# Kernel tuning notes

Measured on AMD Instinct MI355X. Metric: run time of the kernel, lower is better.

## Reference

```python
import jax, jax.numpy as jnp
import numpy as np

B, N, S, C1, C2, CIN, CO = 16, 4096, 1024, 128, 256, 384, 128
BN_EPS = 1e-5


def _bn(x, g, b):
    # BatchNorm1d in training mode: biased batch stats over (B, L) per channel.
    m = x.mean(axis=(0, 1))
    v = x.var(axis=(0, 1))
    return (x - m) * jax.lax.rsqrt(v + BN_EPS) * g + b


def _gelu(x):
    return jax.nn.gelu(x, approximate=False)  # torch nn.GELU default (erf)


def _conv1x1(x, w, b):
    # x: (B, L, Cin), w: (Cout, Cin) -> (B, L, Cout)
    return jnp.einsum('blc,oc->blo', x, w) + b


def setup_inputs() -> dict:
    ks = jax.random.split(jax.random.key(0), 20)
    sc = 0.05
    return {
        'xyz1': jax.random.normal(ks[0], (B, N, 3), jnp.float32),
        'xyz2': jax.random.normal(ks[1], (B, S, 3), jnp.float32),
        'points1': jax.random.normal(ks[2], (B, N, C1), jnp.float32),
        'points2': jax.random.normal(ks[3], (B, S, C2), jnp.float32),
        'fuse_w': jax.random.normal(ks[4], (CO, CIN), jnp.float32) * sc,
        'fuse_b': jax.random.normal(ks[5], (CO,), jnp.float32) * sc,
        'fuse_g': jnp.ones((CO,), jnp.float32),
        'fuse_bt': jnp.zeros((CO,), jnp.float32),
        'w1': jax.random.normal(ks[6], (CO, CO), jnp.float32) * sc,
        'b1': jax.random.normal(ks[7], (CO,), jnp.float32) * sc,
        'g1': jnp.ones((CO,), jnp.float32),
        'bt1': jnp.zeros((CO,), jnp.float32),
        'w2': jax.random.normal(ks[8], (CO, CO), jnp.float32) * sc,
        'b2': jax.random.normal(ks[9], (CO,), jnp.float32) * sc,
        'g2': jnp.ones((CO,), jnp.float32),
        'bt2': jnp.zeros((CO,), jnp.float32),
    }


def reference(xyz1, xyz2, points1, points2,
              fuse_w, fuse_b, fuse_g, fuse_bt,
              w1, b1, g1, bt1, w2, b2, g2, bt2):
    # pairwise euclidean distances (B, N, S) without (B,N,S,3) intermediate
    sq = (jnp.sum(xyz1 * xyz1, -1)[:, :, None]
          + jnp.sum(xyz2 * xyz2, -1)[:, None, :]
          - 2.0 * jnp.einsum('bnd,bsd->bns', xyz1, xyz2))
    dists = jnp.sqrt(jnp.maximum(sq, 1e-12))
    # 3 nearest neighbors, ascending distance
    neg_d3, idx = jax.lax.top_k(-dists, 3)        # (B, N, 3)
    d3 = -neg_d3
    dist_recip = 1.0 / (d3 + 1e-8)
    weight = dist_recip / jnp.sum(dist_recip, axis=-1, keepdims=True)
    gathered = points2[jnp.arange(B)[:, None, None], idx]  # (B, N, 3, C2)
    interp = jnp.sum(gathered * weight[..., None], axis=2)  # (B, N, C2)

    new_points = jnp.concatenate([points1, interp], axis=-1)  # (B, N, CIN)
    x = _gelu(_bn(_conv1x1(new_points, fuse_w, fuse_b), fuse_g, fuse_bt))
    # ConvBNReLURes1D block (groups=1, res_expansion=1.0)
    h = _gelu(_bn(_conv1x1(x, w1, b1), g1, bt1))
    h = _bn(_conv1x1(h, w2, b2), g2, bt2)
    return _gelu(h + x)  # (B, N, CO)
```

## Files before the change

kernel.cpp:

```cpp
#include <hip/hip_runtime.h>
#include <hip/hip_bf16.h>
#include <math.h>

#define B_   16
#define N_   4096
#define S_   1024
#define C1_  128
#define C2_  256
#define CIN_ 384
#define CO_  128
#define ROWS (B_ * N_)

typedef __attribute__((ext_vector_type(8))) __bf16 bf16x8;
typedef __attribute__((ext_vector_type(8))) short  s16x8;
typedef __attribute__((ext_vector_type(4))) short  s16x4;
typedef __attribute__((ext_vector_type(4))) float  f32x4;

__device__ inline float bf2f(short s) {
  unsigned u = ((unsigned)(unsigned short)s) << 16;
  float f; __builtin_memcpy(&f, &u, 4); return f;
}
__device__ inline short f2bf(float f) {
  __hip_bfloat16 h = __float2bfloat16(f);
  short s; __builtin_memcpy(&s, &h, 2); return s;
}
__device__ inline float gelu_f(float v) {
  return 0.5f * v * (1.f + erff(v * 0.70710678118654752f));
}
__device__ inline f32x4 mfma_bf16(s16x8 a, s16x8 b, f32x4 c) {
  return __builtin_amdgcn_mfma_f32_16x16x32_bf16(
      __builtin_bit_cast(bf16x8, a), __builtin_bit_cast(bf16x8, b), c, 0, 0, 0);
}
__device__ inline s16x8 pack8(f32x4 a, f32x4 b) {
  s16x8 r;
  #pragma unroll
  for (int j = 0; j < 4; ++j) { r[j] = f2bf(a[j]); r[j+4] = f2bf(b[j]); }
  return r;
}

__global__ __launch_bounds__(256) void prep_kernel(
    const float* __restrict__ fw, const float* __restrict__ w1,
    const float* __restrict__ w2, short* __restrict__ fwb,
    short* __restrict__ w1b, short* __restrict__ w2b, float* __restrict__ stats)
{
  int i = blockIdx.x * 256 + threadIdx.x;
  if (i < CO_ * CIN_) fwb[i] = f2bf(fw[i]);
  if (i < CO_ * CO_) { w1b[i] = f2bf(w1[i]); w2b[i] = f2bf(w2[i]); }
  if (i < 768) stats[i] = 0.f;
}

__global__ __launch_bounds__(256) void knn_kernel(
    const float* __restrict__ xyz1, const float* __restrict__ xyz2,
    int* __restrict__ idxs, float* __restrict__ wts)
{
  __shared__ float4 pts[S_];
  const int b = blockIdx.y;
  const float* pp = xyz2 + (size_t)b * S_ * 3;
  for (int j = threadIdx.x; j < S_; j += 256) {
    float x = pp[j*3+0], y = pp[j*3+1], z = pp[j*3+2];
    pts[j] = make_float4(x, y, z, x*x + y*y + z*z);
  }
  __syncthreads();
  const int t   = blockIdx.x * 256 + threadIdx.x;
  const int n   = t >> 3;
  const int sub = t & 7;
  const float* q = xyz1 + ((size_t)b * N_ + n) * 3;
  const float qx = q[0], qy = q[1], qz = q[2];
  const float qq = qx*qx + qy*qy + qz*qz;

  float d0 = 3.4e38f, d1 = 3.4e38f, d2 = 3.4e38f;
  int   i0 = 0, i1 = 0, i2 = 0;
  auto ins = [&](float d, int i) {
    bool c2 = d < d2;  d2 = c2 ? d : d2;  i2 = c2 ? i : i2;
    bool c1 = d2 < d1; float td = d1; int ti = i1;
    d1 = c1 ? d2 : d1; i1 = c1 ? i2 : i1;
    d2 = c1 ? td : d2; i2 = c1 ? ti : i2;
    bool c0 = d1 < d0; td = d0; ti = i0;
    d0 = c0 ? d1 : d0; i0 = c0 ? i1 : i0;
    d1 = c0 ? td : d1; i1 = c0 ? ti : i1;
  };
  #pragma unroll 4
  for (int it = 0; it < S_ / 8; ++it) {
    int j = it * 8 + sub;
    float4 p = pts[j];
    float dot = fmaf(qz, p.z, fmaf(qy, p.y, qx * p.x));
    float d = fmaf(-2.f, dot, p.w);
    ins(d, j);
  }
  #pragma unroll
  for (int delta = 1; delta < 8; delta <<= 1) {
    float e0 = __shfl_xor(d0, delta), e1 = __shfl_xor(d1, delta), e2 = __shfl_xor(d2, delta);
    int   j0 = __shfl_xor(i0, delta), j1 = __shfl_xor(i1, delta), j2 = __shfl_xor(i2, delta);
    ins(e0, j0); ins(e1, j1); ins(e2, j2);
  }
  if (sub == 0) {
    float r0 = 1.f / (sqrtf(fmaxf(d0 + qq, 1e-12f)) + 1e-8f);
    float r1 = 1.f / (sqrtf(fmaxf(d1 + qq, 1e-12f)) + 1e-8f);
    float r2 = 1.f / (sqrtf(fmaxf(d2 + qq, 1e-12f)) + 1e-8f);
    float rs = 1.f / (r0 + r1 + r2);
    size_t o = ((size_t)b * N_ + n) * 3;
    idxs[o+0] = i0; idxs[o+1] = i1; idxs[o+2] = i2;
    wts [o+0] = r0*rs; wts[o+1] = r1*rs; wts[o+2] = r2*rs;
  }
}

__device__ inline void epilogue_store_stats(
    f32x4 (&acc)[8][2], int row0, int l16, int lk,
    short* __restrict__ Raw, float* __restrict__ ssum, float* __restrict__ ssq)
{
  #pragma unroll
  for (int m = 0; m < 8; ++m) {
    f32x4 sv = acc[m][0] + acc[m][1];
    f32x4 qv = acc[m][0]*acc[m][0] + acc[m][1]*acc[m][1];
    #pragma unroll
    for (int r = 0; r < 4; ++r) {
      float s = sv[r], q = qv[r];
      s += __shfl_xor(s, 1); q += __shfl_xor(q, 1);
      s += __shfl_xor(s, 2); q += __shfl_xor(q, 2);
      s += __shfl_xor(s, 4); q += __shfl_xor(q, 4);
      s += __shfl_xor(s, 8); q += __shfl_xor(q, 8);
      if (l16 == 0) {
        int c = m*16 + lk*4 + r;
        atomicAdd(&ssum[c], s); atomicAdd(&ssq[c], q);
      }
    }
    #pragma unroll
    for (int nf = 0; nf < 2; ++nf) {
      s16x4 pv;
      #pragma unroll
      for (int r = 0; r < 4; ++r) pv[r] = f2bf(acc[m][nf][r]);
      *(s16x4*)(Raw + (size_t)(row0 + nf*16 + l16) * CO_ + m*16 + lk*4) = pv;
    }
  }
}

__global__ __launch_bounds__(256) void gemm1_fused_kernel(
    const float* __restrict__ p1, const float* __restrict__ p2,
    const int* __restrict__ idxs, const float* __restrict__ wts,
    const short* __restrict__ W, short* __restrict__ Raw,
    float* __restrict__ gsum, float* __restrict__ gsq)
{
  const int tid  = threadIdx.x;
  const int wave = tid >> 6, lane = tid & 63;
  const int l16  = lane & 15, lk = lane >> 4;
  const int row0 = blockIdx.x * 128 + wave * 32;

  __shared__ float ssum[CO_], ssq[CO_];
  if (tid < CO_) { ssum[tid] = 0.f; ssq[tid] = 0.f; }

  const int r0 = row0 + l16, r1 = r0 + 16;
  const int bb = row0 >> 12;
  const float* p2b = p2 + (size_t)bb * S_ * C2_;
  const float* ga0 = p2b + (size_t)idxs[(size_t)r0*3+0] * C2_;
  const float* ga1 = p2b + (size_t)idxs[(size_t)r0*3+1] * C2_;
  const float* ga2 = p2b + (size_t)idxs[(size_t)r0*3+2] * C2_;
  const float  wa0 = wts[(size_t)r0*3+0], wa1 = wts[(size_t)r0*3+1], wa2 = wts[(size_t)r0*3+2];
  const float* gb0 = p2b + (size_t)idxs[(size_t)r1*3+0] * C2_;
  const float* gb1 = p2b + (size_t)idxs[(size_t)r1*3+1] * C2_;
  const float* gb2 = p2b + (size_t)idxs[(size_t)r1*3+2] * C2_;
  const float  wb0 = wts[(size_t)r1*3+0], wb1 = wts[(size_t)r1*3+1], wb2 = wts[(size_t)r1*3+2];

  f32x4 acc[8][2];
  #pragma unroll
  for (int m = 0; m < 8; ++m)
    #pragma unroll
    for (int nf = 0; nf < 2; ++nf) acc[m][nf] = f32x4{0.f,0.f,0.f,0.f};

  const short* wbase = W + (size_t)l16 * CIN_ + lk * 8;
  const float* p1r0  = p1 + (size_t)r0 * C1_ + lk * 8;
  const float* p1r1  = p1 + (size_t)r1 * C1_ + lk * 8;

  #pragma unroll
  for (int kk = 0; kk < 128; kk += 32) {
    s16x8 bf0 = pack8(*(const f32x4*)(p1r0 + kk), *(const f32x4*)(p1r0 + kk + 4));
    s16x8 bf1 = pack8(*(const f32x4*)(p1r1 + kk), *(const f32x4*)(p1r1 + kk + 4));
    #pragma unroll
    for (int m = 0; m < 8; ++m) {
      s16x8 wf = *(const s16x8*)(wbase + (size_t)m*16*CIN_ + kk);
      acc[m][0] = mfma_bf16(wf, bf0, acc[m][0]);
      acc[m][1] = mfma_bf16(wf, bf1, acc[m][1]);
    }
  }
  #pragma unroll 4
  for (int kk2 = 0; kk2 < 256; kk2 += 32) {
    const int c = kk2 + lk * 8;
    f32x4 v0a = wa0 * *(const f32x4*)(ga0 + c)     + wa1 * *(const f32x4*)(ga1 + c)     + wa2 * *(const f32x4*)(ga2 + c);
    f32x4 v0b = wa0 * *(const f32x4*)(ga0 + c + 4) + wa1 * *(const f32x4*)(ga1 + c + 4) + wa2 * *(const f32x4*)(ga2 + c + 4);
    f32x4 v1a = wb0 * *(const f32x4*)(gb0 + c)     + wb1 * *(const f32x4*)(gb1 + c)     + wb2 * *(const f32x4*)(gb2 + c);
    f32x4 v1b = wb0 * *(const f32x4*)(gb0 + c + 4) + wb1 * *(const f32x4*)(gb1 + c + 4) + wb2 * *(const f32x4*)(gb2 + c + 4);
    s16x8 bf0 = pack8(v0a, v0b);
    s16x8 bf1 = pack8(v1a, v1b);
    #pragma unroll
    for (int m = 0; m < 8; ++m) {
      s16x8 wf = *(const s16x8*)(wbase + (size_t)m*16*CIN_ + 128 + kk2);
      acc[m][0] = mfma_bf16(wf, bf0, acc[m][0]);
      acc[m][1] = mfma_bf16(wf, bf1, acc[m][1]);
    }
  }

  __syncthreads();
  epilogue_store_stats(acc, row0, l16, lk, Raw, ssum, ssq);
  __syncthreads();
  if (tid < CO_)      atomicAdd(&gsum[tid],       ssum[tid]);
  else                atomicAdd(&gsq[tid - CO_],  ssq[tid - CO_]);
}

template<int K>
__global__ __launch_bounds__(256) void gemm_bn_kernel(
    const short* __restrict__ A, const short* __restrict__ W,
    short* __restrict__ Raw, float* __restrict__ gsum, float* __restrict__ gsq)
{
  const int tid  = threadIdx.x;
  const int wave = tid >> 6, lane = tid & 63;
  const int l16  = lane & 15, lk = lane >> 4;
  const int row0 = blockIdx.x * 128 + wave * 32;

  __shared__ float ssum[CO_], ssq[CO_];
  if (tid < CO_) { ssum[tid] = 0.f; ssq[tid] = 0.f; }

  f32x4 acc[8][2];
  #pragma unroll
  for (int m = 0; m < 8; ++m)
    #pragma unroll
    for (int nf = 0; nf < 2; ++nf) acc[m][nf] = f32x4{0.f,0.f,0.f,0.f};

  const short* a0    = A + (size_t)(row0 + l16) * K + lk * 8;
  const short* a1    = a0 + (size_t)16 * K;
  const short* wbase = W + (size_t)l16 * K + lk * 8;

  #pragma unroll 4
  for (int kk = 0; kk < K; kk += 32) {
    s16x8 bf0 = *(const s16x8*)(a0 + kk);
    s16x8 bf1 = *(const s16x8*)(a1 + kk);
    #pragma unroll
    for (int m = 0; m < 8; ++m) {
      s16x8 wf = *(const s16x8*)(wbase + (size_t)m*16*K + kk);
      acc[m][0] = mfma_bf16(wf, bf0, acc[m][0]);
      acc[m][1] = mfma_bf16(wf, bf1, acc[m][1]);
    }
  }

  __syncthreads();
  epilogue_store_stats(acc, row0, l16, lk, Raw, ssum, ssq);
  __syncthreads();
  if (tid < CO_)      atomicAdd(&gsum[tid],       ssum[tid]);
  else                atomicAdd(&gsq[tid - CO_],  ssq[tid - CO_]);
}

template<bool FINAL>
__global__ __launch_bounds__(256) void bn_act_kernel(
    const short* __restrict__ raw, const float* __restrict__ gsum,
    const float* __restrict__ gsq, const float* __restrict__ gamma,
    const float* __restrict__ beta, const short* __restrict__ xres,
    void* __restrict__ outp)
{
  __shared__ float ssc[CO_], ssh[CO_];
  const int tid = threadIdx.x;
  if (tid < CO_) {
    const float inv = 1.f / (float)ROWS;
    float mean = gsum[tid] * inv;
    float var  = gsq[tid] * inv - mean * mean;
    float sc   = gamma[tid] * rsqrtf(var + 1e-5f);
    ssc[tid] = sc;
    ssh[tid] = beta[tid] - mean * sc;
  }
  __syncthreads();
  const int gid = blockIdx.x * 256 + tid;
  float sc[8], sh[8];
  const int cpos = (gid & 15) * 8;
  #pragma unroll
  for (int j = 0; j < 8; ++j) { sc[j] = ssc[cpos + j]; sh[j] = ssh[cpos + j]; }
  const int NCHUNK = ROWS * CO_ / 8;
  const int stride = gridDim.x * 256;
  for (int ch = gid; ch < NCHUNK; ch += stride) {
    s16x8 rv = ((const s16x8*)raw)[ch];
    if (!FINAL) {
      s16x8 ov;
      #pragma unroll
      for (int j = 0; j < 8; ++j)
        ov[j] = f2bf(gelu_f(bf2f(rv[j]) * sc[j] + sh[j]));
      ((s16x8*)outp)[ch] = ov;
    } else {
      s16x8 xv = ((const s16x8*)xres)[ch];
      f32x4 o0, o1;
      #pragma unroll
      for (int j = 0; j < 4; ++j)
        o0[j] = gelu_f(bf2f(rv[j]) * sc[j] + sh[j] + bf2f(xv[j]));
      #pragma unroll
      for (int j = 0; j < 4; ++j)
        o1[j] = gelu_f(bf2f(rv[j+4]) * sc[j+4] + sh[j+4] + bf2f(xv[j+4]));
      ((f32x4*)outp)[2*(size_t)ch]     = o0;
      ((f32x4*)outp)[2*(size_t)ch + 1] = o1;
    }
  }
}

extern "C" void kernel_launch(void* const* d_in, const int* in_sizes, int n_in,
                              void* d_out, int out_size, void* d_ws, size_t ws_size,
                              hipStream_t stream) {
  const float* xyz1    = (const float*)d_in[0];
  const float* xyz2    = (const float*)d_in[1];
  const float* points1 = (const float*)d_in[2];
  const float* points2 = (const float*)d_in[3];
  const float* fuse_w  = (const float*)d_in[4];
  const float* fuse_g  = (const float*)d_in[6];
  const float* fuse_bt = (const float*)d_in[7];
  const float* w1      = (const float*)d_in[8];
  const float* g1      = (const float*)d_in[10];
  const float* bt1     = (const float*)d_in[11];
  const float* w2      = (const float*)d_in[12];
  const float* g2      = (const float*)d_in[14];
  const float* bt2     = (const float*)d_in[15];

  char* ws = (char*)d_ws;
  short* x_b   = (short*)(ws);
  short* h_b   = (short*)(ws + 16777216);
  short* raw   = (short*)(ws + 33554432);
  short* wf_b  = (short*)(ws + 50331648);
  short* w1_b  = (short*)(ws + 50429952);
  short* w2_b  = (short*)(ws + 50462720);
  int*   idxs  = (int*)  (ws + 50495488);
  float* wts   = (float*)(ws + 51281920);
  float* stats = (float*)(ws + 52068352);
  float *sum1 = stats,       *sq1 = stats + 128;
  float *sum2 = stats + 256, *sq2 = stats + 384;
  float *sum3 = stats + 512, *sq3 = stats + 640;

  prep_kernel<<<192, 256, 0, stream>>>(fuse_w, w1, w2, wf_b, w1_b, w2_b, stats);
  knn_kernel<<<dim3(N_*8/256, B_), 256, 0, stream>>>(xyz1, xyz2, idxs, wts);

  gemm1_fused_kernel<<<ROWS/128, 256, 0, stream>>>(points1, points2, idxs, wts,
                                                   wf_b, raw, sum1, sq1);
  bn_act_kernel<false><<<2048, 256, 0, stream>>>(raw, sum1, sq1, fuse_g, fuse_bt, nullptr, x_b);

  gemm_bn_kernel<CO_><<<ROWS/128, 256, 0, stream>>>(x_b, w1_b, raw, sum2, sq2);
  bn_act_kernel<false><<<2048, 256, 0, stream>>>(raw, sum2, sq2, g1, bt1, nullptr, h_b);

  gemm_bn_kernel<CO_><<<ROWS/128, 256, 0, stream>>>(h_b, w2_b, raw, sum3, sq3);
  bn_act_kernel<true><<<2048, 256, 0, stream>>>(raw, sum3, sq3, g2, bt2, x_b, d_out);
}
```

Baseline: 311.5 us.

## Stage interpolated features and GEMM weights in swizzled LDS panels

In the fused first GEMM, each wave now gathers the three neighbour rows of points2 with fully coalesced row-wide loads, blends them, and writes bf16 results into an XOR-swizzled shared-memory panel. The MFMA loop then reads B fragments from that panel instead of doing scattered per-lane gathers. The 128x128 GEMM kernels also preload the weight matrix into a swizzled LDS tile, so repeated global weight loads inside the K loop are replaced by LDS reads. The trade-off is 64KB of LDS per block in gemm1, which may lower occupancy, plus an extra barrier and a serial prologue to fill the panel.

```diff
diff --git a/kernel.cpp b/kernel.cpp
--- a/kernel.cpp
+++ b/kernel.cpp
@@ -35,6 +35,12 @@
   s16x8 r;
   #pragma unroll
   for (int j = 0; j < 4; ++j) { r[j] = f2bf(a[j]); r[j+4] = f2bf(b[j]); }
+  return r;
+}
+__device__ inline s16x4 pack4(f32x4 a) {
+  s16x4 r;
+  #pragma unroll
+  for (int j = 0; j < 4; ++j) r[j] = f2bf(a[j]);
   return r;
 }
 
@@ -106,7 +112,7 @@
 
 __device__ inline void epilogue_store_stats(
     f32x4 (&acc)[8][2], int row0, int l16, int lk,
-    short* __restrict__ Raw, float* __restrict__ ssum, float* __restrict__ ssq)
+    short* Raw, float* ssum, float* ssq)
 {
   #pragma unroll
   for (int m = 0; m < 8; ++m) {
@@ -126,9 +132,7 @@
     }
     #pragma unroll
     for (int nf = 0; nf < 2; ++nf) {
-      s16x4 pv;
-      #pragma unroll
-      for (int r = 0; r < 4; ++r) pv[r] = f2bf(acc[m][nf][r]);
+      s16x4 pv = pack4(acc[m][nf]);
       *(s16x4*)(Raw + (size_t)(row0 + nf*16 + l16) * CO_ + m*16 + lk*4) = pv;
     }
   }
@@ -140,25 +144,53 @@
     const short* __restrict__ W, short* __restrict__ Raw,
     float* __restrict__ gsum, float* __restrict__ gsq)
 {
+  __shared__ short ipan[128][256];
+  float* ssum = (float*)&ipan[0][0];
+  float* ssq  = ssum + CO_;
+
   const int tid  = threadIdx.x;
   const int wave = tid >> 6, lane = tid & 63;
   const int l16  = lane & 15, lk = lane >> 4;
   const int row0 = blockIdx.x * 128 + wave * 32;
-
-  __shared__ float ssum[CO_], ssq[CO_];
-  if (tid < CO_) { ssum[tid] = 0.f; ssq[tid] = 0.f; }
-
-  const int r0 = row0 + l16, r1 = r0 + 16;
-  const int bb = row0 >> 12;
+  const int rowB = blockIdx.x * 128;
+  const int bb   = rowB >> 12;
   const float* p2b = p2 + (size_t)bb * S_ * C2_;
-  const float* ga0 = p2b + (size_t)idxs[(size_t)r0*3+0] * C2_;
-  const float* ga1 = p2b + (size_t)idxs[(size_t)r0*3+1] * C2_;
-  const float* ga2 = p2b + (size_t)idxs[(size_t)r0*3+2] * C2_;
-  const float  wa0 = wts[(size_t)r0*3+0], wa1 = wts[(size_t)r0*3+1], wa2 = wts[(size_t)r0*3+2];
-  const float* gb0 = p2b + (size_t)idxs[(size_t)r1*3+0] * C2_;
-  const float* gb1 = p2b + (size_t)idxs[(size_t)r1*3+1] * C2_;
-  const float* gb2 = p2b + (size_t)idxs[(size_t)r1*3+2] * C2_;
-  const float  wb0 = wts[(size_t)r1*3+0], wb1 = wts[(size_t)r1*3+1], wb2 = wts[(size_t)r1*3+2];
+
+  {
+    const int wr0 = wave * 32;
+    int   ni0, ni1, ni2;  float nw0, nw1, nw2;
+    int   mi0, mi1, mi2;  float mw0, mw1, mw2;
+    {
+      size_t g0 = (size_t)(rowB + wr0) * 3, g1 = (size_t)(rowB + wr0 + 1) * 3;
+      ni0 = idxs[g0]; ni1 = idxs[g0+1]; ni2 = idxs[g0+2];
+      nw0 = wts[g0];  nw1 = wts[g0+1];  nw2 = wts[g0+2];
+      mi0 = idxs[g1]; mi1 = idxs[g1+1]; mi2 = idxs[g1+2];
+      mw0 = wts[g1];  mw1 = wts[g1+1];  mw2 = wts[g1+2];
+    }
+    for (int j = 0; j < 32; j += 2) {
+      f32x4 a0 = *(const f32x4*)(p2b + (size_t)ni0 * C2_ + lane*4);
+      f32x4 a1 = *(const f32x4*)(p2b + (size_t)ni1 * C2_ + lane*4);
+      f32x4 a2 = *(const f32x4*)(p2b + (size_t)ni2 * C2_ + lane*4);
+      f32x4 b0 = *(const f32x4*)(p2b + (size_t)mi0 * C2_ + lane*4);
+      f32x4 b1 = *(const f32x4*)(p2b + (size_t)mi1 * C2_ + lane*4);
+      f32x4 b2 = *(const f32x4*)(p2b + (size_t)mi2 * C2_ + lane*4);
+      float cw0 = nw0, cw1 = nw1, cw2 = nw2;
+      float dw0 = mw0, dw1 = mw1, dw2 = mw2;
+      if (j < 30) {
+        size_t g0 = (size_t)(rowB + wr0 + j + 2) * 3, g1 = (size_t)(rowB + wr0 + j + 3) * 3;
+        ni0 = idxs[g0]; ni1 = idxs[g0+1]; ni2 = idxs[g0+2];
+        nw0 = wts[g0];  nw1 = wts[g0+1];  nw2 = wts[g0+2];
+        mi0 = idxs[g1]; mi1 = idxs[g1+1]; mi2 = idxs[g1+2];
+        mw0 = wts[g1];  mw1 = wts[g1+1];  mw2 = wts[g1+2];
+      }
+      f32x4 va = cw0*a0 + cw1*a1 + cw2*a2;
+      f32x4 vb = dw0*b0 + dw1*b1 + dw2*b2;
+      char* r0p = (char*)&ipan[wr0 + j][0];
+      char* r1p = (char*)&ipan[wr0 + j + 1][0];
+      *(s16x4*)(r0p + ((lane*8) ^ (( j      & 7) << 4))) = pack4(va);
+      *(s16x4*)(r1p + ((lane*8) ^ (((j + 1) & 7) << 4))) = pack4(vb);
+    }
+  }
 
   f32x4 acc[8][2];
   #pragma unroll
@@ -167,13 +199,13 @@
     for (int nf = 0; nf < 2; ++nf) acc[m][nf] = f32x4{0.f,0.f,0.f,0.f};
 
   const short* wbase = W + (size_t)l16 * CIN_ + lk * 8;
-  const float* p1r0  = p1 + (size_t)r0 * C1_ + lk * 8;
-  const float* p1r1  = p1 + (size_t)r1 * C1_ + lk * 8;
+  const float* pr0   = p1 + (size_t)(row0 + l16) * C1_ + lk * 8;
+  const float* pr1   = pr0 + (size_t)16 * C1_;
 
   #pragma unroll
   for (int kk = 0; kk < 128; kk += 32) {
-    s16x8 bf0 = pack8(*(const f32x4*)(p1r0 + kk), *(const f32x4*)(p1r0 + kk + 4));
-    s16x8 bf1 = pack8(*(const f32x4*)(p1r1 + kk), *(const f32x4*)(p1r1 + kk + 4));
+    s16x8 bf0 = pack8(*(const f32x4*)(pr0 + kk), *(const f32x4*)(pr0 + kk + 4));
+    s16x8 bf1 = pack8(*(const f32x4*)(pr1 + kk), *(const f32x4*)(pr1 + kk + 4));
     #pragma unroll
     for (int m = 0; m < 8; ++m) {
       s16x8 wf = *(const s16x8*)(wbase + (size_t)m*16*CIN_ + kk);
@@ -181,23 +213,26 @@
       acc[m][1] = mfma_bf16(wf, bf1, acc[m][1]);
     }
   }
-  #pragma unroll 4
-  for (int kk2 = 0; kk2 < 256; kk2 += 32) {
-    const int c = kk2 + lk * 8;
-    f32x4 v0a = wa0 * *(const f32x4*)(ga0 + c)     + wa1 * *(const f32x4*)(ga1 + c)     + wa2 * *(const f32x4*)(ga2 + c);
-    f32x4 v0b = wa0 * *(const f32x4*)(ga0 + c + 4) + wa1 * *(const f32x4*)(ga1 + c + 4) + wa2 * *(const f32x4*)(ga2 + c + 4);
-    f32x4 v1a = wb0 * *(const f32x4*)(gb0 + c)     + wb1 * *(const f32x4*)(gb1 + c)     + wb2 * *(const f32x4*)(gb2 + c);
-    f32x4 v1b = wb0 * *(const f32x4*)(gb0 + c + 4) + wb1 * *(const f32x4*)(gb1 + c + 4) + wb2 * *(const f32x4*)(gb2 + c + 4);
-    s16x8 bf0 = pack8(v0a, v0b);
-    s16x8 bf1 = pack8(v1a, v1b);
-    #pragma unroll
-    for (int m = 0; m < 8; ++m) {
-      s16x8 wf = *(const s16x8*)(wbase + (size_t)m*16*CIN_ + 128 + kk2);
-      acc[m][0] = mfma_bf16(wf, bf0, acc[m][0]);
-      acc[m][1] = mfma_bf16(wf, bf1, acc[m][1]);
-    }
-  }
-
+  {
+    const char* ip0 = (const char*)&ipan[wave*32 + l16][0];
+    const char* ip1 = ip0 + 16 * 512;
+    const int   swz = (l16 & 7) << 4;
+    #pragma unroll 4
+    for (int cc = 0; cc < 8; ++cc) {
+      s16x8 bf0 = *(const s16x8*)(ip0 + ((cc*64 + lk*16) ^ swz));
+      s16x8 bf1 = *(const s16x8*)(ip1 + ((cc*64 + lk*16) ^ swz));
+      #pragma unroll
+      for (int m = 0; m < 8; ++m) {
+        s16x8 wf = *(const s16x8*)(wbase + (size_t)m*16*CIN_ + 128 + cc*32);
+        acc[m][0] = mfma_bf16(wf, bf0, acc[m][0]);
+        acc[m][1] = mfma_bf16(wf, bf1, acc[m][1]);
+      }
+    }
+  }
+
+  __syncthreads();
+  if (tid < CO_) ssum[tid] = 0.f;
+  else if (tid < 2*CO_) ssq[tid - CO_] = 0.f;
   __syncthreads();
   epilogue_store_stats(acc, row0, l16, lk, Raw, ssum, ssq);
   __syncthreads();
@@ -205,18 +240,28 @@
   else                atomicAdd(&gsq[tid - CO_],  ssq[tid - CO_]);
 }
 
-template<int K>
 __global__ __launch_bounds__(256) void gemm_bn_kernel(
     const short* __restrict__ A, const short* __restrict__ W,
     short* __restrict__ Raw, float* __restrict__ gsum, float* __restrict__ gsq)
 {
+  __shared__ short wpan[CO_][128];
+  __shared__ float ssum[CO_], ssq[CO_];
+
   const int tid  = threadIdx.x;
   const int wave = tid >> 6, lane = tid & 63;
   const int l16  = lane & 15, lk = lane >> 4;
   const int row0 = blockIdx.x * 128 + wave * 32;
 
-  __shared__ float ssum[CO_], ssq[CO_];
   if (tid < CO_) { ssum[tid] = 0.f; ssq[tid] = 0.f; }
+  #pragma unroll
+  for (int i = 0; i < 8; ++i) {
+    const int Ls  = i * 2048 + tid * 8;
+    const int row = Ls >> 7;
+    const int cb  = (Ls & 127) * 2;
+    s16x8 v = *(const s16x8*)(W + Ls);
+    *(s16x8*)((char*)&wpan[row][0] + (cb ^ ((row & 7) << 4))) = v;
+  }
+  __syncthreads();
 
   f32x4 acc[8][2];
   #pragma unroll
@@ -224,17 +269,18 @@
     #pragma unroll
     for (int nf = 0; nf < 2; ++nf) acc[m][nf] = f32x4{0.f,0.f,0.f,0.f};
 
-  const short* a0    = A + (size_t)(row0 + l16) * K + lk * 8;
-  const short* a1    = a0 + (size_t)16 * K;
-  const short* wbase = W + (size_t)l16 * K + lk * 8;
-
-  #pragma unroll 4
-  for (int kk = 0; kk < K; kk += 32) {
-    s16x8 bf0 = *(const s16x8*)(a0 + kk);
-    s16x8 bf1 = *(const s16x8*)(a1 + kk);
+  const short* a0 = A + (size_t)(row0 + l16) * CO_ + lk * 8;
+  const short* a1 = a0 + (size_t)16 * CO_;
+  const int swz = (l16 & 7) << 4;
+
+  #pragma unroll
+  for (int kc = 0; kc < 4; ++kc) {
+    s16x8 bf0 = *(const s16x8*)(a0 + kc*32);
+    s16x8 bf1 = *(const s16x8*)(a1 + kc*32);
     #pragma unroll
     for (int m = 0; m < 8; ++m) {
-      s16x8 wf = *(const s16x8*)(wbase + (size_t)m*16*K + kk);
+      const char* wp = (const char*)&wpan[m*16 + l16][0];
+      s16x8 wf = *(const s16x8*)(wp + ((kc*64 + lk*16) ^ swz));
       acc[m][0] = mfma_bf16(wf, bf0, acc[m][0]);
       acc[m][1] = mfma_bf16(wf, bf1, acc[m][1]);
     }
@@ -333,9 +379,9 @@
                                                    wf_b, raw, sum1, sq1);
   bn_act_kernel<false><<<2048, 256, 0, stream>>>(raw, sum1, sq1, fuse_g, fuse_bt, nullptr, x_b);
 
-  gemm_bn_kernel<CO_><<<ROWS/128, 256, 0, stream>>>(x_b, w1_b, raw, sum2, sq2);
+  gemm_bn_kernel<<<ROWS/128, 256, 0, stream>>>(x_b, w1_b, raw, sum2, sq2);
   bn_act_kernel<false><<<2048, 256, 0, stream>>>(raw, sum2, sq2, g1, bt1, nullptr, h_b);
 
-  gemm_bn_kernel<CO_><<<ROWS/128, 256, 0, stream>>>(h_b, w2_b, raw, sum3, sq3);
+  gemm_bn_kernel<<<ROWS/128, 256, 0, stream>>>(h_b, w2_b, raw, sum3, sq3);
   bn_act_kernel<true><<<2048, 256, 0, stream>>>(raw, sum3, sq3, g2, bt2, x_b, d_out);
 }
```

Result: faster. 294.2 us (-5.6%).

## Split interpolation into bf16 pack kernel and stage GEMM tiles through LDS

Applied to the files above, without the earlier changes.

The interpolation and concatenation move out of the first GEMM into a separate kernel that writes a bf16 new_points buffer. All three 1x1-conv GEMMs then share one kernel that stages A and W tiles into swizzled LDS with global_load_lds before feeding MFMA. This is meant to replace scattered per-wave global loads of weights and gathered rows with coalesced, reusable LDS tiles. The cost is an extra round trip of a large intermediate buffer through HBM and a bigger workspace footprint.

```diff
diff --git a/kernel.cpp b/kernel.cpp
--- a/kernel.cpp
+++ b/kernel.cpp
@@ -31,11 +31,16 @@
   return __builtin_amdgcn_mfma_f32_16x16x32_bf16(
       __builtin_bit_cast(bf16x8, a), __builtin_bit_cast(bf16x8, b), c, 0, 0, 0);
 }
-__device__ inline s16x8 pack8(f32x4 a, f32x4 b) {
-  s16x8 r;
-  #pragma unroll
-  for (int j = 0; j < 4; ++j) { r[j] = f2bf(a[j]); r[j+4] = f2bf(b[j]); }
+__device__ inline s16x4 pack4(f32x4 a) {
+  s16x4 r;
+  #pragma unroll
+  for (int j = 0; j < 4; ++j) r[j] = f2bf(a[j]);
   return r;
+}
+__device__ inline void gload16(const void* g, void* l) {
+  __builtin_amdgcn_global_load_lds(
+      (const __attribute__((address_space(1))) void*)g,
+      (__attribute__((address_space(3))) void*)l, 16, 0, 0);
 }
 
 __global__ __launch_bounds__(256) void prep_kernel(
@@ -104,10 +109,103 @@
   }
 }
 
-__device__ inline void epilogue_store_stats(
-    f32x4 (&acc)[8][2], int row0, int l16, int lk,
-    short* __restrict__ Raw, float* __restrict__ ssum, float* __restrict__ ssq)
-{
+__global__ __launch_bounds__(256) void interp_pack_kernel(
+    const float* __restrict__ p1, const float* __restrict__ p2,
+    const int* __restrict__ idxs, const float* __restrict__ wts,
+    short* __restrict__ np)
+{
+  const int gw   = (blockIdx.x * 256 + threadIdx.x) >> 6;
+  const int lane = threadIdx.x & 63;
+  const int rbase = gw * 8;
+  const int b = rbase >> 12;
+  const float* p2b = p2 + (size_t)b * S_ * C2_;
+  #pragma unroll
+  for (int u = 0; u < 4; ++u) {
+    const int r0 = rbase + u*2, r1 = r0 + 1;
+    size_t m0 = (size_t)r0*3, m1 = (size_t)r1*3;
+    int ia0=idxs[m0], ia1=idxs[m0+1], ia2=idxs[m0+2];
+    int ib0=idxs[m1], ib1=idxs[m1+1], ib2=idxs[m1+2];
+    float wa0=wts[m0], wa1=wts[m0+1], wa2=wts[m0+2];
+    float wb0=wts[m1], wb1=wts[m1+1], wb2=wts[m1+2];
+    float2 pa = *(const float2*)(p1 + (size_t)r0*C1_ + lane*2);
+    float2 pb = *(const float2*)(p1 + (size_t)r1*C1_ + lane*2);
+    f32x4 a0 = *(const f32x4*)(p2b + (size_t)ia0*C2_ + lane*4);
+    f32x4 a1 = *(const f32x4*)(p2b + (size_t)ia1*C2_ + lane*4);
+    f32x4 a2 = *(const f32x4*)(p2b + (size_t)ia2*C2_ + lane*4);
+    f32x4 c0 = *(const f32x4*)(p2b + (size_t)ib0*C2_ + lane*4);
+    f32x4 c1 = *(const f32x4*)(p2b + (size_t)ib1*C2_ + lane*4);
+    f32x4 c2 = *(const f32x4*)(p2b + (size_t)ib2*C2_ + lane*4);
+    f32x4 va = wa0*a0 + wa1*a1 + wa2*a2;
+    f32x4 vb = wb0*c0 + wb1*c1 + wb2*c2;
+    short* o0 = np + (size_t)r0 * CIN_;
+    short* o1 = np + (size_t)r1 * CIN_;
+    unsigned pk0 = (unsigned)(unsigned short)f2bf(pa.x) | ((unsigned)(unsigned short)f2bf(pa.y) << 16);
+    unsigned pk1 = (unsigned)(unsigned short)f2bf(pb.x) | ((unsigned)(unsigned short)f2bf(pb.y) << 16);
+    *(unsigned*)(o0 + lane*2) = pk0;
+    *(unsigned*)(o1 + lane*2) = pk1;
+    *(s16x4*)(o0 + C1_ + lane*4) = pack4(va);
+    *(s16x4*)(o1 + C1_ + lane*4) = pack4(vb);
+  }
+}
+
+template<int K>
+__global__ __launch_bounds__(256) void gemm_bn_kernel(
+    const short* __restrict__ A, const short* __restrict__ W,
+    short* __restrict__ Raw, float* __restrict__ gsum, float* __restrict__ gsq)
+{
+  __shared__ char Atile[16384];
+  __shared__ char Wtile[16384];
+  __shared__ float ssum[CO_], ssq[CO_];
+
+  const int tid  = threadIdx.x;
+  const int wave = tid >> 6, lane = tid & 63;
+  const int l16  = lane & 15, lk = lane >> 4;
+  const int row0 = blockIdx.x * 128;
+
+  if (tid < CO_) { ssum[tid] = 0.f; ssq[tid] = 0.f; }
+
+  f32x4 acc[8][2];
+  #pragma unroll
+  for (int m = 0; m < 8; ++m)
+    #pragma unroll
+    for (int nf = 0; nf < 2; ++nf) acc[m][nf] = f32x4{0.f,0.f,0.f,0.f};
+
+  int srow[4], soff[4];
+  #pragma unroll
+  for (int i = 0; i < 4; ++i) {
+    int L = i*4096 + tid*16;
+    int row = L >> 7;
+    int slot = ((L >> 4) & 7) ^ (row & 7);
+    srow[i] = row; soff[i] = slot * 16;
+  }
+  const int ra = wave*32 + l16, rb = ra + 16;
+  #pragma unroll
+  for (int kt = 0; kt < K/64; ++kt) {
+    const int kb = kt * 128;
+    #pragma unroll
+    for (int i = 0; i < 4; ++i) {
+      gload16((const char*)A + (size_t)(row0 + srow[i])*(K*2) + kb + soff[i],
+              Atile + i*4096 + tid*16);
+      gload16((const char*)W + (size_t)srow[i]*(K*2) + kb + soff[i],
+              Wtile + i*4096 + tid*16);
+    }
+    __syncthreads();
+    #pragma unroll
+    for (int kc = 0; kc < 2; ++kc) {
+      const int s = kc*4 + lk;
+      s16x8 bf0 = *(const s16x8*)(Atile + ra*128 + ((s ^ (ra & 7)) * 16));
+      s16x8 bf1 = *(const s16x8*)(Atile + rb*128 + ((s ^ (rb & 7)) * 16));
+      #pragma unroll
+      for (int m = 0; m < 8; ++m) {
+        const int rw = m*16 + l16;
+        s16x8 wf = *(const s16x8*)(Wtile + rw*128 + ((s ^ (rw & 7)) * 16));
+        acc[m][0] = mfma_bf16(wf, bf0, acc[m][0]);
+        acc[m][1] = mfma_bf16(wf, bf1, acc[m][1]);
+      }
+    }
+    __syncthreads();
+  }
+
   #pragma unroll
   for (int m = 0; m < 8; ++m) {
     f32x4 sv = acc[m][0] + acc[m][1];
@@ -126,122 +224,10 @@
     }
     #pragma unroll
     for (int nf = 0; nf < 2; ++nf) {
-      s16x4 pv;
-      #pragma unroll
-      for (int r = 0; r < 4; ++r) pv[r] = f2bf(acc[m][nf][r]);
-      *(s16x4*)(Raw + (size_t)(row0 + nf*16 + l16) * CO_ + m*16 + lk*4) = pv;
-    }
-  }
-}
-
-__global__ __launch_bounds__(256) void gemm1_fused_kernel(
-    const float* __restrict__ p1, const float* __restrict__ p2,
-    const int* __restrict__ idxs, const float* __restrict__ wts,
-    const short* __restrict__ W, short* __restrict__ Raw,
-    float* __restrict__ gsum, float* __restrict__ gsq)
-{
-  const int tid  = threadIdx.x;
-  const int wave = tid >> 6, lane = tid & 63;
-  const int l16  = lane & 15, lk = lane >> 4;
-  const int row0 = blockIdx.x * 128 + wave * 32;
-
-  __shared__ float ssum[CO_], ssq[CO_];
-  if (tid < CO_) { ssum[tid] = 0.f; ssq[tid] = 0.f; }
-
-  const int r0 = row0 + l16, r1 = r0 + 16;
-  const int bb = row0 >> 12;
-  const float* p2b = p2 + (size_t)bb * S_ * C2_;
-  const float* ga0 = p2b + (size_t)idxs[(size_t)r0*3+0] * C2_;
-  const float* ga1 = p2b + (size_t)idxs[(size_t)r0*3+1] * C2_;
-  const float* ga2 = p2b + (size_t)idxs[(size_t)r0*3+2] * C2_;
-  const float  wa0 = wts[(size_t)r0*3+0], wa1 = wts[(size_t)r0*3+1], wa2 = wts[(size_t)r0*3+2];
-  const float* gb0 = p2b + (size_t)idxs[(size_t)r1*3+0] * C2_;
-  const float* gb1 = p2b + (size_t)idxs[(size_t)r1*3+1] * C2_;
-  const float* gb2 = p2b + (size_t)idxs[(size_t)r1*3+2] * C2_;
-  const float  wb0 = wts[(size_t)r1*3+0], wb1 = wts[(size_t)r1*3+1], wb2 = wts[(size_t)r1*3+2];
-
-  f32x4 acc[8][2];
-  #pragma unroll
-  for (int m = 0; m < 8; ++m)
-    #pragma unroll
-    for (int nf = 0; nf < 2; ++nf) acc[m][nf] = f32x4{0.f,0.f,0.f,0.f};
-
-  const short* wbase = W + (size_t)l16 * CIN_ + lk * 8;
-  const float* p1r0  = p1 + (size_t)r0 * C1_ + lk * 8;
-  const float* p1r1  = p1 + (size_t)r1 * C1_ + lk * 8;
-
-  #pragma unroll
-  for (int kk = 0; kk < 128; kk += 32) {
-    s16x8 bf0 = pack8(*(const f32x4*)(p1r0 + kk), *(const f32x4*)(p1r0 + kk + 4));
-    s16x8 bf1 = pack8(*(const f32x4*)(p1r1 + kk), *(const f32x4*)(p1r1 + kk + 4));
-    #pragma unroll
-    for (int m = 0; m < 8; ++m) {
-      s16x8 wf = *(const s16x8*)(wbase + (size_t)m*16*CIN_ + kk);
-      acc[m][0] = mfma_bf16(wf, bf0, acc[m][0]);
-      acc[m][1] = mfma_bf16(wf, bf1, acc[m][1]);
-    }
-  }
-  #pragma unroll 4
-  for (int kk2 = 0; kk2 < 256; kk2 += 32) {
-    const int c = kk2 + lk * 8;
-    f32x4 v0a = wa0 * *(const f32x4*)(ga0 + c)     + wa1 * *(const f32x4*)(ga1 + c)     + wa2 * *(const f32x4*)(ga2 + c);
-    f32x4 v0b = wa0 * *(const f32x4*)(ga0 + c + 4) + wa1 * *(const f32x4*)(ga1 + c + 4) + wa2 * *(const f32x4*)(ga2 + c + 4);
-    f32x4 v1a = wb0 * *(const f32x4*)(gb0 + c)     + wb1 * *(const f32x4*)(gb1 + c)     + wb2 * *(const f32x4*)(gb2 + c);
-    f32x4 v1b = wb0 * *(const f32x4*)(gb0 + c + 4) + wb1 * *(const f32x4*)(gb1 + c + 4) + wb2 * *(const f32x4*)(gb2 + c + 4);
-    s16x8 bf0 = pack8(v0a, v0b);
-    s16x8 bf1 = pack8(v1a, v1b);
-    #pragma unroll
-    for (int m = 0; m < 8; ++m) {
-      s16x8 wf = *(const s16x8*)(wbase + (size_t)m*16*CIN_ + 128 + kk2);
-      acc[m][0] = mfma_bf16(wf, bf0, acc[m][0]);
-      acc[m][1] = mfma_bf16(wf, bf1, acc[m][1]);
-    }
-  }
-
-  __syncthreads();
-  epilogue_store_stats(acc, row0, l16, lk, Raw, ssum, ssq);
-  __syncthreads();
-  if (tid < CO_)      atomicAdd(&gsum[tid],       ssum[tid]);
-  else                atomicAdd(&gsq[tid - CO_],  ssq[tid - CO_]);
-}
-
-template<int K>
-__global__ __launch_bounds__(256) void gemm_bn_kernel(
-    const short* __restrict__ A, const short* __restrict__ W,
-    short* __restrict__ Raw, float* __restrict__ gsum, float* __restrict__ gsq)
-{
-  const int tid  = threadIdx.x;
-  const int wave = tid >> 6, lane = tid & 63;
-  const int l16  = lane & 15, lk = lane >> 4;
-  const int row0 = blockIdx.x * 128 + wave * 32;
-
-  __shared__ float ssum[CO_], ssq[CO_];
-  if (tid < CO_) { ssum[tid] = 0.f; ssq[tid] = 0.f; }
-
-  f32x4 acc[8][2];
-  #pragma unroll
-  for (int m = 0; m < 8; ++m)
-    #pragma unroll
-    for (int nf = 0; nf < 2; ++nf) acc[m][nf] = f32x4{0.f,0.f,0.f,0.f};
-
-  const short* a0    = A + (size_t)(row0 + l16) * K + lk * 8;
-  const short* a1    = a0 + (size_t)16 * K;
-  const short* wbase = W + (size_t)l16 * K + lk * 8;
-
-  #pragma unroll 4
-  for (int kk = 0; kk < K; kk += 32) {
-    s16x8 bf0 = *(const s16x8*)(a0 + kk);
-    s16x8 bf1 = *(const s16x8*)(a1 + kk);
-    #pragma unroll
-    for (int m = 0; m < 8; ++m) {
-      s16x8 wf = *(const s16x8*)(wbase + (size_t)m*16*K + kk);
-      acc[m][0] = mfma_bf16(wf, bf0, acc[m][0]);
-      acc[m][1] = mfma_bf16(wf, bf1, acc[m][1]);
-    }
-  }
-
-  __syncthreads();
-  epilogue_store_stats(acc, row0, l16, lk, Raw, ssum, ssq);
+      s16x4 pv = pack4(acc[m][nf]);
+      *(s16x4*)(Raw + (size_t)(row0 + wave*32 + nf*16 + l16) * CO_ + m*16 + lk*4) = pv;
+    }
+  }
   __syncthreads();
   if (tid < CO_)      atomicAdd(&gsum[tid],       ssum[tid]);
   else                atomicAdd(&gsq[tid - CO_],  ssq[tid - CO_]);
@@ -313,24 +299,25 @@
   const float* bt2     = (const float*)d_in[15];
 
   char* ws = (char*)d_ws;
+  short* np_b  = (short*)(ws);
   short* x_b   = (short*)(ws);
   short* h_b   = (short*)(ws + 16777216);
-  short* raw   = (short*)(ws + 33554432);
-  short* wf_b  = (short*)(ws + 50331648);
-  short* w1_b  = (short*)(ws + 50429952);
-  short* w2_b  = (short*)(ws + 50462720);
-  int*   idxs  = (int*)  (ws + 50495488);
-  float* wts   = (float*)(ws + 51281920);
-  float* stats = (float*)(ws + 52068352);
+  short* raw   = (short*)(ws + 50331648);
+  short* wf_b  = (short*)(ws + 67108864);
+  short* w1_b  = (short*)(ws + 67207168);
+  short* w2_b  = (short*)(ws + 67239936);
+  int*   idxs  = (int*)  (ws + 67272704);
+  float* wts   = (float*)(ws + 68059136);
+  float* stats = (float*)(ws + 68845568);
   float *sum1 = stats,       *sq1 = stats + 128;
   float *sum2 = stats + 256, *sq2 = stats + 384;
   float *sum3 = stats + 512, *sq3 = stats + 640;
 
   prep_kernel<<<192, 256, 0, stream>>>(fuse_w, w1, w2, wf_b, w1_b, w2_b, stats);
   knn_kernel<<<dim3(N_*8/256, B_), 256, 0, stream>>>(xyz1, xyz2, idxs, wts);
-
-  gemm1_fused_kernel<<<ROWS/128, 256, 0, stream>>>(points1, points2, idxs, wts,
-                                                   wf_b, raw, sum1, sq1);
+  interp_pack_kernel<<<2048, 256, 0, stream>>>(points1, points2, idxs, wts, np_b);
+
+  gemm_bn_kernel<CIN_><<<ROWS/128, 256, 0, stream>>>(np_b, wf_b, raw, sum1, sq1);
   bn_act_kernel<false><<<2048, 256, 0, stream>>>(raw, sum1, sq1, fuse_g, fuse_bt, nullptr, x_b);
 
   gemm_bn_kernel<CO_><<<ROWS/128, 256, 0, stream>>>(x_b, w1_b, raw, sum2, sq2);
```

Result: faster. 289.6 us (-7.0%).
